# Performance work log

Measured on AMD Instinct MI355X. Metric: run time of the kernel, lower is better.

## Reference

```python
import jax, jax.numpy as jnp
import numpy as np

D_MODEL = 1024
D_INNER = 1024
N_HEADS = 16
D_HEAD = D_INNER // N_HEADS
B = 2
CUR = 1024
PREV = 1024
LN_EPS = 1e-5


def _rel_shift(x):
    # x: (b, i, j, h) -- faithful to torch: pad along i, flat-reinterpret, drop first row
    b, i, j, h = x.shape
    zp = jnp.zeros((b, 1, j, h), x.dtype)
    xp = jnp.concatenate([zp, x], axis=1).reshape(i + 1, b, j, h)
    return xp[1:].reshape(b, i, j, h)


def setup_inputs() -> dict:
    key = jax.random.key(0)
    ks = jax.random.split(key, 10)
    x = jax.random.normal(ks[0], (B, CUR, D_MODEL), jnp.float32)
    mem = jax.random.normal(ks[1], (B, PREV, D_MODEL), jnp.float32)
    pos_emb = jax.random.normal(ks[2], (CUR + PREV, D_INNER), jnp.float32)
    u = jax.random.normal(ks[3], (N_HEADS, D_HEAD), jnp.float32) * 0.02
    v = jax.random.normal(ks[4], (N_HEADS, D_HEAD), jnp.float32) * 0.02
    # causal mask: query i (current segment) may attend key j if j <= i + PREV
    idx_i = jnp.arange(CUR)[:, None]
    idx_j = jnp.arange(CUR + PREV)[None, :]
    tgt_mask = jnp.broadcast_to((idx_j > idx_i + PREV)[None, :, :, None], (B, CUR, CUR + PREV, 1))
    Wq = jax.random.normal(ks[5], (D_INNER, D_MODEL), jnp.float32) * 0.02
    Wkv = jax.random.normal(ks[6], (2 * D_INNER, D_MODEL), jnp.float32) * 0.02
    Wfc = jax.random.normal(ks[7], (D_MODEL, D_INNER), jnp.float32) * 0.02
    bfc = jnp.zeros((D_MODEL,), jnp.float32)
    gamma = jnp.ones((D_MODEL,), jnp.float32)
    beta = jnp.zeros((D_MODEL,), jnp.float32)
    return {"x": x, "pos_emb": pos_emb, "u": u, "v": v, "mem": mem,
            "tgt_mask": tgt_mask, "Wq": Wq, "Wkv": Wkv, "Wfc": Wfc,
            "bfc": bfc, "gamma": gamma, "beta": beta}


def reference(x, pos_emb, u, v, mem, tgt_mask, Wq, Wkv, Wfc, bfc, gamma, beta):
    b, cur, _ = x.shape
    prev = mem.shape[1]
    tot = cur + prev
    h_telda = jnp.concatenate([mem, x], axis=1)               # (b, tot, d_model)
    q = jnp.einsum('bsm,im->bsi', x, Wq)                      # (b, cur, d_inner)
    kv = jnp.einsum('bsm,im->bsi', h_telda, Wkv)              # (b, tot, 2*d_inner)
    k, vv = kv[..., :D_INNER], kv[..., D_INNER:]
    q = q.reshape(b, cur, N_HEADS, D_HEAD)
    k = k.reshape(b, tot, N_HEADS, D_HEAD)
    vv = vv.reshape(b, tot, N_HEADS, D_HEAD)
    content = jnp.einsum('bihd,bjhd->bijh', q + u, k)
    pos = pos_emb.reshape(tot, N_HEADS, D_HEAD)
    pos_attn = jnp.einsum('bihd,jhd->bijh', q + v, pos)
    attn = content + _rel_shift(pos_attn)
    attn = jnp.where(tgt_mask, -jnp.inf, attn)
    attn = attn / (D_HEAD ** 0.5)
    attn = jax.nn.softmax(attn, axis=1)  # faithful: softmax over query dim as in original
    out = jnp.einsum('bijh,bjhd->bihd', attn, vv).reshape(b, cur, D_INNER)
    y = x + jnp.einsum('bsi,mi->bsm', out, Wfc) + bfc
    mu = jnp.mean(y, axis=-1, keepdims=True)
    var = jnp.mean((y - mu) ** 2, axis=-1, keepdims=True)
    return (y - mu) / jnp.sqrt(var + LN_EPS) * gamma + beta
```

## Files before the change

kernel.cpp:

```cpp
#include <hip/hip_runtime.h>
#include <hip/hip_bf16.h>
#include <stdint.h>

typedef unsigned short u16;
typedef __attribute__((ext_vector_type(8))) __bf16 bf16x8;
typedef __attribute__((ext_vector_type(4))) float f32x4;
typedef __attribute__((ext_vector_type(4))) float float4v;
typedef __attribute__((ext_vector_type(4))) u16  u16x4;
typedef __attribute__((ext_vector_type(8))) u16  u16x8;

#define DEV __device__ __forceinline__

#define NB   2
#define CUR  1024
#define PREV 1024
#define TOT  2048
#define DM   1024
#define NH   16
#define DH   64

DEV u16 f2b(float f) {
    uint32_t u = __builtin_bit_cast(uint32_t, f);
    uint32_t r = (u + 0x7fffu + ((u >> 16) & 1u)) >> 16;
    return (u16)r;
}
DEV float b2f(u16 u) {
    return __builtin_bit_cast(float, (uint32_t)u << 16);
}

typedef const __attribute__((address_space(1))) void* gptr_t;
typedef __attribute__((address_space(3))) void*       lptr_t;
DEV void async16(const void* g, void* l) {
    __builtin_amdgcn_global_load_lds((gptr_t)g, (lptr_t)l, 16, 0, 0);
}

template<int BM, int BN, int BK, int WM, int WN, int EPI>
__global__ __launch_bounds__(256)
void gemm_bt(const u16* __restrict__ A, const u16* __restrict__ B,
             int M, int N, int K, long sA, long sB, int bzBase,
             void* __restrict__ C0, void* __restrict__ C1,
             const float* __restrict__ F0, const float* __restrict__ F1)
{
    constexpr int WAVES_N = BN / WN;
    constexpr int MI = WM / 16, NI = WN / 16;
    static_assert((BM / WM) * (BN / WN) == 4, "4 waves");
    static_assert(BK == 64, "swizzle assumes 8 chunks/row");

    __shared__ u16 lA[BM * BK];
    __shared__ u16 lB[BN * BK];

    const int bz = blockIdx.z;
    const int m0 = blockIdx.y * BM, n0 = blockIdx.x * BN;
    const int tid = threadIdx.x, wave = tid >> 6, lane = tid & 63;

    const u16* Ab = A + (long)bz * sA;
    const u16* Bb = B + (long)bz * sB;
    const int wm0 = (wave / WAVES_N) * WM, wn0 = (wave % WAVES_N) * WN;
    const int quad = lane >> 4;

    f32x4 acc[MI][NI];
#pragma unroll
    for (int mi = 0; mi < MI; ++mi)
#pragma unroll
        for (int ni = 0; ni < NI; ++ni)
            acc[mi][ni] = f32x4{0.f, 0.f, 0.f, 0.f};

    const int srow = tid >> 3;
    const int ksw  = (((tid & 7) ^ ((tid >> 3) & 7)) << 3);

    for (int kt = 0; kt < K; kt += BK) {
        __syncthreads();
#pragma unroll
        for (int is = 0; is < (BM * BK) / 2048; ++is) {
            int r = is * 32 + srow;
            async16(Ab + (long)(m0 + r) * K + kt + ksw, &lA[is * 2048 + wave * 512]);
        }
#pragma unroll
        for (int is = 0; is < (BN * BK) / 2048; ++is) {
            int r = is * 32 + srow;
            async16(Bb + (long)(n0 + r) * K + kt + ksw, &lB[is * 2048 + wave * 512]);
        }
        __syncthreads();
#pragma unroll
        for (int ks = 0; ks < BK; ks += 32) {
            bf16x8 af[MI], br[NI];
#pragma unroll
            for (int mi = 0; mi < MI; ++mi)
                af[mi] = *(const bf16x8*)(const void*)
                    &lA[(wm0 + mi * 16 + (lane & 15)) * BK +
                        ((((ks >> 3) + quad) ^ (lane & 7)) << 3)];
#pragma unroll
            for (int ni = 0; ni < NI; ++ni)
                br[ni] = *(const bf16x8*)(const void*)
                    &lB[(wn0 + ni * 16 + (lane & 15)) * BK +
                        ((((ks >> 3) + quad) ^ (lane & 7)) << 3)];
#pragma unroll
            for (int mi = 0; mi < MI; ++mi)
#pragma unroll
                for (int ni = 0; ni < NI; ++ni)
                    acc[mi][ni] = __builtin_amdgcn_mfma_f32_16x16x32_bf16(af[mi], br[ni], acc[mi][ni], 0, 0, 0);
        }
    }

    const int gbz = bzBase + bz;

    if constexpr (EPI == 1) {
        u16* Abuf = (u16*)C0;
        const int b = gbz;
#pragma unroll
        for (int mi = 0; mi < MI; ++mi) {
            const int m = m0 + wm0 + mi * 16 + quad * 4;
            const int h = m >> 6, d = m & 63;
            const float4v uu = *(const float4v*)(F0 + m);
            const float4v vv = *(const float4v*)(F1 + m);
#pragma unroll
            for (int ni = 0; ni < NI; ++ni) {
                const int i = n0 + wn0 + ni * 16 + (lane & 15);
                u16x4 pu, pv;
#pragma unroll
                for (int r = 0; r < 4; ++r) {
                    pu[r] = f2b(acc[mi][ni][r] + uu[r]);
                    pv[r] = f2b(acc[mi][ni][r] + vv[r]);
                }
                *(u16x4*)(Abuf + (((long)(b * NH + h)) * CUR + i) * 128 + d) = pu;
                if (b == 0) {
                    if (i > 0)
                        *(u16x4*)(Abuf + (((long)h) * CUR + (i - 1)) * 128 + 64 + d) = pv;
                    if (i == 1023) {
                        u16x4 z = {};
                        *(u16x4*)(Abuf + (((long)h) * CUR + 1023) * 128 + 64 + d) = z;
                    }
                } else {
                    *(u16x4*)(Abuf + (((long)(NH + h)) * CUR + i) * 128 + 64 + d) = pv;
                }
            }
        }
    } else if constexpr (EPI == 2) {
#pragma unroll
        for (int mi = 0; mi < MI; ++mi) {
            const int m = m0 + wm0 + mi * 16 + quad * 4;
            const bool isV = m >= DM;
            const int h = (m >> 6) & 15, d = m & 63;
#pragma unroll
            for (int ni = 0; ni < NI; ++ni) {
                const int n = n0 + wn0 + ni * 16 + (lane & 15);
                const int b = n >> 11, j = n & 2047;
                u16x4 p;
#pragma unroll
                for (int r = 0; r < 4; ++r) p[r] = f2b(acc[mi][ni][r]);
                if (!isV)
                    *(u16x4*)((u16*)C0 + (((long)(b * NH + h)) * TOT + j) * 128 + d) = p;
                else
                    *(u16x4*)((u16*)C1 + (((long)(b * NH + h)) * TOT + j) * 64 + d) = p;
            }
        }
    } else if constexpr (EPI == 5) {
#pragma unroll
        for (int mi = 0; mi < MI; ++mi) {
            const int m = m0 + wm0 + mi * 16 + quad * 4;
            const float4v bb = *(const float4v*)(F1 + m);
#pragma unroll
            for (int ni = 0; ni < NI; ++ni) {
                const int n = n0 + wn0 + ni * 16 + (lane & 15);
                const float4v xr = *(const float4v*)(F0 + (long)n * DM + m);
                float4v y;
#pragma unroll
                for (int r = 0; r < 4; ++r) y[r] = xr[r] + acc[mi][ni][r] + bb[r];
                *(float4v*)((float*)C0 + (long)n * DM + m) = y;
            }
        }
    }
}

template<int DO_PV>
__global__ __launch_bounds__(256, 2)
void attn2(const u16* __restrict__ Abuf, const u16* __restrict__ Bbuf,
           const u16* __restrict__ Vp, float* __restrict__ colsum,
           u16* __restrict__ Opart)
{
    __shared__ u16 lQ[64 * 128];
    __shared__ float lO[DO_PV ? 64 * 68 : 1];

    const int id  = blockIdx.x;
    const int xcd = id & 7;
    const int wi  = id >> 3;
    const int bh  = xcd + ((wi >> 5) << 3);
    const int rem = wi & 31;
    const int it  = 15 - (rem & 15);
    const int ch  = rem >> 4;

    const int n0 = it * 64;
    const int tid = threadIdx.x, wave = tid >> 6, lane = tid & 63;
    const int l15 = lane & 15, quad = lane >> 4;

    const u16* Qg = Abuf + ((long)bh * CUR + n0) * 128;
    const u16* Kg = Bbuf + (long)bh * TOT * 128;
    const u16* Vg = Vp + (long)bh * DH * TOT;
    float* CS = colsum + (long)bh * TOT;

    {
        const int r4 = tid >> 4, c4 = tid & 15;
        const int csQ = (c4 & 8) | ((c4 & 7) ^ (r4 & 7));
#pragma unroll
        for (int is = 0; is < 4; ++is)
            async16(Qg + (long)(is * 16 + r4) * 128 + csQ * 8, &lQ[is * 2048 + wave * 512]);
    }
    __syncthreads();

    f32x4 oacc[4][4];
    if constexpr (DO_PV) {
#pragma unroll
        for (int mi = 0; mi < 4; ++mi)
#pragma unroll
            for (int smi = 0; smi < 4; ++smi)
                oacc[mi][smi] = f32x4{0.f, 0.f, 0.f, 0.f};
    }

    const int jw = wave * 16;
    const int nt = it + 17;
    const int half = (nt + 1) >> 1;
    const int t0 = ch ? half : 0;
    const int t1 = ch ? nt : half;

    for (int t = t0; t < t1; ++t) {
        const int jbase = t * 64 + jw;
        const u16* Krow = Kg + (long)(jbase + l15) * 128 + quad * 8;
        bf16x8 kreg[4];
#pragma unroll
        for (int c = 0; c < 4; ++c)
            kreg[c] = *(const bf16x8*)(const void*)(Krow + c * 32);

        f32x4 sacc[4];
#pragma unroll
        for (int smi = 0; smi < 4; ++smi) sacc[smi] = f32x4{0.f, 0.f, 0.f, 0.f};
#pragma unroll
        for (int c = 0; c < 4; ++c) {
            const int cq = c * 4 + quad;
#pragma unroll
            for (int smi = 0; smi < 4; ++smi) {
                const bf16x8 qf = *(const bf16x8*)(const void*)
                    &lQ[(smi * 16 + l15) * 128 + (((cq & 8) | ((cq & 7) ^ (l15 & 7))) << 3)];
                sacc[smi] = __builtin_amdgcn_mfma_f32_16x16x32_bf16(kreg[c], qf, sacc[smi], 0, 0, 0);
            }
        }

        if constexpr (DO_PV) {
            bf16x8 vf[4];
#pragma unroll
            for (int mi = 0; mi < 4; ++mi) {
                const u16x4 vl = *(const u16x4*)(Vg + (long)(mi * 16 + l15) * TOT + jbase + quad * 4);
                const u16x8 vraw = {vl[0], vl[1], vl[2], vl[3], 0, 0, 0, 0};
                vf[mi] = __builtin_bit_cast(bf16x8, vraw);
            }
#pragma unroll
            for (int smi = 0; smi < 4; ++smi) {
                const int ii = n0 + smi * 16 + l15;
                u16 p0 = 0, p1 = 0, p2 = 0, p3 = 0;
                const int jq = jbase + quad * 4;
                if (jq + 0 <= ii + PREV) p0 = f2b(__expf(sacc[smi][0] * 0.125f));
                if (jq + 1 <= ii + PREV) p1 = f2b(__expf(sacc[smi][1] * 0.125f));
                if (jq + 2 <= ii + PREV) p2 = f2b(__expf(sacc[smi][2] * 0.125f));
                if (jq + 3 <= ii + PREV) p3 = f2b(__expf(sacc[smi][3] * 0.125f));
                const u16x8 praw = {p0, p1, p2, p3, 0, 0, 0, 0};
                const bf16x8 pb = __builtin_bit_cast(bf16x8, praw);
#pragma unroll
                for (int mi = 0; mi < 4; ++mi)
                    oacc[mi][smi] = __builtin_amdgcn_mfma_f32_16x16x32_bf16(vf[mi], pb, oacc[mi][smi], 0, 0, 0);
            }
        } else {
            float cs[4] = {0.f, 0.f, 0.f, 0.f};
            const int jq = jbase + quad * 4;
#pragma unroll
            for (int smi = 0; smi < 4; ++smi) {
                const int ii = n0 + smi * 16 + l15;
#pragma unroll
                for (int r = 0; r < 4; ++r)
                    if (jq + r <= ii + PREV) cs[r] += __expf(sacc[smi][r] * 0.125f);
            }
#pragma unroll
            for (int r = 0; r < 4; ++r) {
                cs[r] += __shfl_xor(cs[r], 1);
                cs[r] += __shfl_xor(cs[r], 2);
                cs[r] += __shfl_xor(cs[r], 4);
                cs[r] += __shfl_xor(cs[r], 8);
            }
            if (l15 == 0) {
                atomicAdd(CS + jq + 0, cs[0]);
                atomicAdd(CS + jq + 1, cs[1]);
                atomicAdd(CS + jq + 2, cs[2]);
                atomicAdd(CS + jq + 3, cs[3]);
            }
        }
    }

    if constexpr (DO_PV) {
#pragma unroll
        for (int wv = 0; wv < 4; ++wv) {
            if (wave == wv) {
#pragma unroll
                for (int mi = 0; mi < 4; ++mi)
#pragma unroll
                    for (int smi = 0; smi < 4; ++smi) {
                        const int i = smi * 16 + l15, d = mi * 16 + quad * 4;
                        float* p = &lO[i * 68 + d];
                        if (wv == 0) *(f32x4*)p = oacc[mi][smi];
                        else {
                            f32x4 cur = *(const f32x4*)p;
#pragma unroll
                            for (int r = 0; r < 4; ++r) cur[r] += oacc[mi][smi][r];
                            *(f32x4*)p = cur;
                        }
                    }
            }
            __syncthreads();
        }
        const int b = bh >> 4, h = bh & 15;
        u16* Ob = Opart + ((long)(ch * NB + b) * CUR) * DM + h * DH;
#pragma unroll
        for (int k2 = 0; k2 < 4; ++k2) {
            const int idx = k2 * 1024 + tid * 4;
            const int il = idx >> 6, d = idx & 63;
            const f32x4 vv = *(const f32x4*)&lO[il * 68 + d];
            u16x4 o;
#pragma unroll
            for (int r = 0; r < 4; ++r) o[r] = f2b(vv[r]);
            *(u16x4*)(Ob + (long)(n0 + il) * DM + d) = o;
        }
    }
}

__global__ __launch_bounds__(256)
void combine_O(const u16* __restrict__ O0, const u16* __restrict__ O1,
               u16* __restrict__ Obf)
{
    int i = blockIdx.x * 256 + threadIdx.x;
    u16x4 a = ((const u16x4*)O0)[i];
    u16x4 c = ((const u16x4*)O1)[i];
    u16x4 o;
#pragma unroll
    for (int r = 0; r < 4; ++r) o[r] = f2b(b2f(a[r]) + b2f(c[r]));
    ((u16x4*)Obf)[i] = o;
}

__global__ __launch_bounds__(256)
void cvt_weights(const float* __restrict__ Wq, const float* __restrict__ Wkv,
                 const float* __restrict__ Wfc, u16* __restrict__ Wqb,
                 u16* __restrict__ Wkvb, u16* __restrict__ Wfcb)
{
    int i = blockIdx.x * 256 + threadIdx.x;
    const float* s; u16* d; int off;
    if (i < 262144)      { s = Wq;  d = Wqb;  off = i; }
    else if (i < 786432) { s = Wkv; d = Wkvb; off = i - 262144; }
    else                 { s = Wfc; d = Wfcb; off = i - 786432; }
    float4v f = ((const float4v*)s)[off];
    u16x4 o = {f2b(f[0]), f2b(f[1]), f2b(f[2]), f2b(f[3])};
    ((u16x4*)d)[off] = o;
}

__global__ __launch_bounds__(256)
void pack_H(const float* __restrict__ mem, const float* __restrict__ x, u16* __restrict__ dst)
{
    int i = blockIdx.x * 256 + threadIdx.x;
    int e = i << 2;
    int b = e >> 21, r = e & ((1 << 21) - 1);
    const float* src = (r < (1 << 20)) ? (mem + ((long)b << 20) + r)
                                       : (x + ((long)b << 20) + (r - (1 << 20)));
    float4v f = *(const float4v*)src;
    u16x4 o = {f2b(f[0]), f2b(f[1]), f2b(f[2]), f2b(f[3])};
    ((u16x4*)dst)[i] = o;
}

__global__ __launch_bounds__(256)
void pack_pos(const float* __restrict__ pos, u16* __restrict__ Bbuf)
{
    int i = blockIdx.x * 256 + threadIdx.x;
    int e = i << 2;
    int h = e >> 17, r = e & 131071, j = r >> 6, d = r & 63;
    float4v f = *(const float4v*)(pos + (long)j * DM + h * DH + d);
    u16x4 o = {f2b(f[0]), f2b(f[1]), f2b(f[2]), f2b(f[3])};
    long base = ((long)h * TOT + j) * 128 + 64 + d;
    *(u16x4*)(Bbuf + base) = o;
    *(u16x4*)(Bbuf + base + (long)NH * TOT * 128) = o;
}

__global__ __launch_bounds__(256)
void vprime_kernel(const u16* __restrict__ Vtmp, const float* __restrict__ colsum,
                   u16* __restrict__ Vp)
{
    __shared__ float t[64][65];
    int bz = blockIdx.y;
    int j0 = blockIdx.x * 64;
    const u16* src = Vtmp + ((long)bz * TOT + j0) * 64;
    const float* cs = colsum + (long)bz * TOT + j0;
    for (int e = threadIdx.x; e < 4096; e += 256) {
        int jl = e >> 6, d = e & 63;
        t[jl][d] = b2f(src[e]) / cs[jl];
    }
    __syncthreads();
    u16* dst = Vp + (long)bz * DH * TOT + j0;
    for (int e = threadIdx.x; e < 4096; e += 256) {
        int d = e >> 6, jl = e & 63;
        dst[(long)d * TOT + jl] = f2b(t[jl][d]);
    }
}

__global__ __launch_bounds__(256)
void ln_kernel(const float* __restrict__ Y, const float* __restrict__ gamma,
               const float* __restrict__ beta, float* __restrict__ out)
{
    const int row = blockIdx.x;
    const float* y = Y + (long)row * DM;
    float v[4];
    float s = 0.f;
#pragma unroll
    for (int t = 0; t < 4; ++t) { v[t] = y[threadIdx.x + t * 256]; s += v[t]; }
#pragma unroll
    for (int off = 32; off > 0; off >>= 1) s += __shfl_down(s, off);
    __shared__ float r1[4], r2[4];
    int wv = threadIdx.x >> 6, ln = threadIdx.x & 63;
    if (ln == 0) r1[wv] = s;
    __syncthreads();
    float mu = (r1[0] + r1[1] + r1[2] + r1[3]) * (1.f / DM);
    float q = 0.f;
#pragma unroll
    for (int t = 0; t < 4; ++t) { float d = v[t] - mu; q += d * d; }
#pragma unroll
    for (int off = 32; off > 0; off >>= 1) q += __shfl_down(q, off);
    if (ln == 0) r2[wv] = q;
    __syncthreads();
    float var = (r2[0] + r2[1] + r2[2] + r2[3]) * (1.f / DM);
    float inv = rsqrtf(var + 1e-5f);
#pragma unroll
    for (int t = 0; t < 4; ++t) {
        int c = threadIdx.x + t * 256;
        out[(long)row * DM + c] = (v[t] - mu) * inv * gamma[c] + beta[c];
    }
}

extern "C" void kernel_launch(void* const* d_in, const int* in_sizes, int n_in,
                              void* d_out, int out_size, void* d_ws, size_t ws_size,
                              hipStream_t stream)
{
    const float* x     = (const float*)d_in[0];
    const float* pos   = (const float*)d_in[1];
    const float* u     = (const float*)d_in[2];
    const float* vbias = (const float*)d_in[3];
    const float* mem   = (const float*)d_in[4];
    const float* Wq    = (const float*)d_in[6];
    const float* Wkv   = (const float*)d_in[7];
    const float* Wfc   = (const float*)d_in[8];
    const float* bfc   = (const float*)d_in[9];
    const float* gamma = (const float*)d_in[10];
    const float* beta  = (const float*)d_in[11];
    float* out = (float*)d_out;

    char* w = (char*)d_ws;
    auto alloc = [&](size_t bytes) {
        char* p = w;
        w += (bytes + 255) & ~(size_t)255;
        return p;
    };
    u16*   Hb     = (u16*)alloc(4096UL * 1024 * 2);
    u16*   Wqb    = (u16*)alloc(1024UL * 1024 * 2);
    u16*   Wkvb   = (u16*)alloc(2048UL * 1024 * 2);
    u16*   Wfcb   = (u16*)alloc(1024UL * 1024 * 2);
    u16*   Abuf   = (u16*)alloc(32UL * 1024 * 128 * 2);
    u16*   Bbuf   = (u16*)alloc(32UL * 2048 * 128 * 2);
    u16*   Vtmp   = (u16*)alloc(32UL * 2048 * 64 * 2);
    u16*   Vp     = (u16*)alloc(32UL * 64 * 2048 * 2);
    float* colsum = (float*)alloc(32UL * 2048 * 4);
    u16*   Opart  = (u16*)alloc(2UL * 2048 * 1024 * 2);
    u16*   Obf    = (u16*)alloc(2048UL * 1024 * 2);
    float* Yf     = (float*)alloc(2048UL * 1024 * 4);

    hipMemsetAsync(colsum, 0, 32UL * 2048 * 4, stream);

    cvt_weights<<<4096, 256, 0, stream>>>(Wq, Wkv, Wfc, Wqb, Wkvb, Wfcb);
    pack_H  <<<4096, 256, 0, stream>>>(mem, x, Hb);
    pack_pos<<<2048, 256, 0, stream>>>(pos, Bbuf);

    gemm_bt<128, 64, 64, 64, 32, 1><<<dim3(16, 8, 2), 256, 0, stream>>>(
        Wqb, Hb + 1024UL * 1024, 1024, 1024, 1024, 0, 2048L * 1024, 0,
        Abuf, nullptr, u, vbias);
    gemm_bt<128, 128, 64, 64, 64, 2><<<dim3(32, 16, 1), 256, 0, stream>>>(
        Wkvb, Hb, 2048, 4096, 1024, 0, 0, 0, Bbuf, Vtmp, nullptr, nullptr);

    attn2<0><<<dim3(1024), 256, 0, stream>>>(
        Abuf, Bbuf, nullptr, colsum, nullptr);
    vprime_kernel<<<dim3(32, 32), 256, 0, stream>>>(Vtmp, colsum, Vp);
    attn2<1><<<dim3(1024), 256, 0, stream>>>(
        Abuf, Bbuf, Vp, nullptr, Opart);
    combine_O<<<2048, 256, 0, stream>>>(Opart, Opart + 2048UL * 1024, Obf);

    gemm_bt<64, 128, 64, 32, 64, 5><<<dim3(16, 16, 1), 256, 0, stream>>>(
        Wfcb, Obf, 1024, 2048, 1024, 0, 0, 0, Yf, nullptr, x, bfc);
    ln_kernel<<<2048, 256, 0, stream>>>(Yf, gamma, beta, out);
}
```

Baseline: 197.8 us.

## Halve attention query tile to 32 rows and hold Q fragments in registers

The attention kernels now process 32 query rows per block instead of 64, which doubles the grid to 2048 blocks, and they load Q fragments straight into registers instead of staging them in LDS. The causal tile count is recomputed at the finer granularity, which trims some masked work, and launch bounds are raised to allow more blocks per CU. The aim is better load balance, higher occupancy and no Q LDS traffic or sync. The cost is that each K/V tile load is reused by only half as many query rows, so global K and V reads roughly double.

```diff
diff --git a/kernel.cpp b/kernel.cpp
--- a/kernel.cpp
+++ b/kernel.cpp
@@ -173,23 +173,22 @@
 }
 
 template<int DO_PV>
-__global__ __launch_bounds__(256, 2)
-void attn2(const u16* __restrict__ Abuf, const u16* __restrict__ Bbuf,
+__global__ __launch_bounds__(256, DO_PV ? 3 : 4)
+void attn3(const u16* __restrict__ Abuf, const u16* __restrict__ Bbuf,
            const u16* __restrict__ Vp, float* __restrict__ colsum,
            u16* __restrict__ Opart)
 {
-    __shared__ u16 lQ[64 * 128];
-    __shared__ float lO[DO_PV ? 64 * 68 : 1];
+    __shared__ float lO[DO_PV ? 32 * 68 : 1];
 
     const int id  = blockIdx.x;
     const int xcd = id & 7;
     const int wi  = id >> 3;
-    const int bh  = xcd + ((wi >> 5) << 3);
-    const int rem = wi & 31;
-    const int it  = 15 - (rem & 15);
-    const int ch  = rem >> 4;
-
-    const int n0 = it * 64;
+    const int bh  = xcd + ((wi >> 6) << 3);
+    const int rem = wi & 63;
+    const int it  = 31 - (rem & 31);
+    const int ch  = rem >> 5;
+
+    const int n0 = it * 32;
     const int tid = threadIdx.x, wave = tid >> 6, lane = tid & 63;
     const int l15 = lane & 15, quad = lane >> 4;
 
@@ -198,26 +197,25 @@
     const u16* Vg = Vp + (long)bh * DH * TOT;
     float* CS = colsum + (long)bh * TOT;
 
-    {
-        const int r4 = tid >> 4, c4 = tid & 15;
-        const int csQ = (c4 & 8) | ((c4 & 7) ^ (r4 & 7));
-#pragma unroll
-        for (int is = 0; is < 4; ++is)
-            async16(Qg + (long)(is * 16 + r4) * 128 + csQ * 8, &lQ[is * 2048 + wave * 512]);
-    }
-    __syncthreads();
-
-    f32x4 oacc[4][4];
+    bf16x8 qreg[4][2];
+#pragma unroll
+    for (int c = 0; c < 4; ++c)
+#pragma unroll
+        for (int smi = 0; smi < 2; ++smi)
+            qreg[c][smi] = *(const bf16x8*)(const void*)
+                (Qg + (long)(smi * 16 + l15) * 128 + (c * 4 + quad) * 8);
+
+    f32x4 oacc[4][2];
     if constexpr (DO_PV) {
 #pragma unroll
         for (int mi = 0; mi < 4; ++mi)
 #pragma unroll
-            for (int smi = 0; smi < 4; ++smi)
+            for (int smi = 0; smi < 2; ++smi)
                 oacc[mi][smi] = f32x4{0.f, 0.f, 0.f, 0.f};
     }
 
     const int jw = wave * 16;
-    const int nt = it + 17;
+    const int nt = ((n0 + 1055) >> 6) + 1;
     const int half = (nt + 1) >> 1;
     const int t0 = ch ? half : 0;
     const int t1 = ch ? nt : half;
@@ -230,33 +228,31 @@
         for (int c = 0; c < 4; ++c)
             kreg[c] = *(const bf16x8*)(const void*)(Krow + c * 32);
 
-        f32x4 sacc[4];
-#pragma unroll
-        for (int smi = 0; smi < 4; ++smi) sacc[smi] = f32x4{0.f, 0.f, 0.f, 0.f};
-#pragma unroll
-        for (int c = 0; c < 4; ++c) {
-            const int cq = c * 4 + quad;
-#pragma unroll
-            for (int smi = 0; smi < 4; ++smi) {
-                const bf16x8 qf = *(const bf16x8*)(const void*)
-                    &lQ[(smi * 16 + l15) * 128 + (((cq & 8) | ((cq & 7) ^ (l15 & 7))) << 3)];
-                sacc[smi] = __builtin_amdgcn_mfma_f32_16x16x32_bf16(kreg[c], qf, sacc[smi], 0, 0, 0);
-            }
-        }
-
+        bf16x8 vf[4];
         if constexpr (DO_PV) {
-            bf16x8 vf[4];
 #pragma unroll
             for (int mi = 0; mi < 4; ++mi) {
                 const u16x4 vl = *(const u16x4*)(Vg + (long)(mi * 16 + l15) * TOT + jbase + quad * 4);
                 const u16x8 vraw = {vl[0], vl[1], vl[2], vl[3], 0, 0, 0, 0};
                 vf[mi] = __builtin_bit_cast(bf16x8, vraw);
             }
-#pragma unroll
-            for (int smi = 0; smi < 4; ++smi) {
+        }
+
+        f32x4 sacc[2];
+#pragma unroll
+        for (int smi = 0; smi < 2; ++smi) sacc[smi] = f32x4{0.f, 0.f, 0.f, 0.f};
+#pragma unroll
+        for (int c = 0; c < 4; ++c)
+#pragma unroll
+            for (int smi = 0; smi < 2; ++smi)
+                sacc[smi] = __builtin_amdgcn_mfma_f32_16x16x32_bf16(kreg[c], qreg[c][smi], sacc[smi], 0, 0, 0);
+
+        if constexpr (DO_PV) {
+#pragma unroll
+            for (int smi = 0; smi < 2; ++smi) {
                 const int ii = n0 + smi * 16 + l15;
+                const int jq = jbase + quad * 4;
                 u16 p0 = 0, p1 = 0, p2 = 0, p3 = 0;
-                const int jq = jbase + quad * 4;
                 if (jq + 0 <= ii + PREV) p0 = f2b(__expf(sacc[smi][0] * 0.125f));
                 if (jq + 1 <= ii + PREV) p1 = f2b(__expf(sacc[smi][1] * 0.125f));
                 if (jq + 2 <= ii + PREV) p2 = f2b(__expf(sacc[smi][2] * 0.125f));
@@ -271,7 +267,7 @@
             float cs[4] = {0.f, 0.f, 0.f, 0.f};
             const int jq = jbase + quad * 4;
 #pragma unroll
-            for (int smi = 0; smi < 4; ++smi) {
+            for (int smi = 0; smi < 2; ++smi) {
                 const int ii = n0 + smi * 16 + l15;
 #pragma unroll
                 for (int r = 0; r < 4; ++r)
@@ -300,7 +296,7 @@
 #pragma unroll
                 for (int mi = 0; mi < 4; ++mi)
 #pragma unroll
-                    for (int smi = 0; smi < 4; ++smi) {
+                    for (int smi = 0; smi < 2; ++smi) {
                         const int i = smi * 16 + l15, d = mi * 16 + quad * 4;
                         float* p = &lO[i * 68 + d];
                         if (wv == 0) *(f32x4*)p = oacc[mi][smi];
@@ -317,7 +313,7 @@
         const int b = bh >> 4, h = bh & 15;
         u16* Ob = Opart + ((long)(ch * NB + b) * CUR) * DM + h * DH;
 #pragma unroll
-        for (int k2 = 0; k2 < 4; ++k2) {
+        for (int k2 = 0; k2 < 2; ++k2) {
             const int idx = k2 * 1024 + tid * 4;
             const int il = idx >> 6, d = idx & 63;
             const f32x4 vv = *(const f32x4*)&lO[il * 68 + d];
@@ -485,10 +481,10 @@
     gemm_bt<128, 128, 64, 64, 64, 2><<<dim3(32, 16, 1), 256, 0, stream>>>(
         Wkvb, Hb, 2048, 4096, 1024, 0, 0, 0, Bbuf, Vtmp, nullptr, nullptr);
 
-    attn2<0><<<dim3(1024), 256, 0, stream>>>(
+    attn3<0><<<dim3(2048), 256, 0, stream>>>(
         Abuf, Bbuf, nullptr, colsum, nullptr);
     vprime_kernel<<<dim3(32, 32), 256, 0, stream>>>(Vtmp, colsum, Vp);
-    attn2<1><<<dim3(1024), 256, 0, stream>>>(
+    attn3<1><<<dim3(2048), 256, 0, stream>>>(
         Abuf, Bbuf, Vp, nullptr, Opart);
     combine_O<<<2048, 256, 0, stream>>>(Opart, Opart + 2048UL * 1024, Obf);
 
```

After: 297.2 us. 50.3% more time.
